# Performance work log

Measured on AMD Instinct MI355X. Metric: run time of the kernel, lower is better.

## Reference

```python
import jax, jax.numpy as jnp
import numpy as np

B, T, D, H, O = 64, 512, 64, 512, 64

def setup_inputs() -> dict:
    key = jax.random.key(0)
    ks = jax.random.split(key, 12)
    s = lambda fan: 1.0 / np.sqrt(fan)
    return {
        "x": jax.random.normal(ks[0], (B, T, D), jnp.float32),
        "W_ih0": jax.random.normal(ks[1], (4 * H, D), jnp.float32) * s(D),
        "W_hh0": jax.random.normal(ks[2], (4 * H, H), jnp.float32) * s(H),
        "b_ih0": jax.random.normal(ks[3], (4 * H,), jnp.float32) * s(H),
        "b_hh0": jax.random.normal(ks[4], (4 * H,), jnp.float32) * s(H),
        "W_ih1": jax.random.normal(ks[5], (4 * H, H), jnp.float32) * s(H),
        "W_hh1": jax.random.normal(ks[6], (4 * H, H), jnp.float32) * s(H),
        "b_ih1": jax.random.normal(ks[7], (4 * H,), jnp.float32) * s(H),
        "b_hh1": jax.random.normal(ks[8], (4 * H,), jnp.float32) * s(H),
        "lin_w": jax.random.normal(ks[9], (O, H), jnp.float32) * s(H),
        "lin_b": jax.random.normal(ks[10], (O,), jnp.float32) * s(H),
    }

def _lstm_layer(x_seq, h0, c0, W_ih, W_hh, b_ih, b_hh):
    # Precompute input contribution for all timesteps: [B, T, 4H]
    xg = jnp.einsum('btd,gd->btg', x_seq, W_ih) + b_ih
    def step(carry, xg_t):
        h, c = carry
        gates = xg_t + h @ W_hh.T + b_hh  # [B, 4H]
        i, f, g, o = jnp.split(gates, 4, axis=-1)
        i = jax.nn.sigmoid(i); f = jax.nn.sigmoid(f)
        g = jnp.tanh(g); o = jax.nn.sigmoid(o)
        c = f * c + i * g  # eval mode: dropout mask is identity
        h = o * jnp.tanh(c)
        return (h, c), h
    (h, c), ys = jax.lax.scan(step, (h0, c0), jnp.swapaxes(xg, 0, 1))
    return jnp.swapaxes(ys, 0, 1), h, c

def reference(x, W_ih0, W_hh0, b_ih0, b_hh0, W_ih1, W_hh1, b_ih1, b_hh1, lin_w, lin_b):
    h = jnp.zeros((x.shape[0], H), x.dtype)
    c = jnp.zeros((x.shape[0], H), x.dtype)
    # NOTE: faithful to source — h/c are only zeroed before layer 0 and
    # carried into layer 1 as its initial state.
    y0, h, c = _lstm_layer(x, h, c, W_ih0, W_hh0, b_ih0, b_hh0)
    y1, h, c = _lstm_layer(y0, h, c, W_ih1, W_hh1, b_ih1, b_hh1)
    return h @ lin_w.T + lin_b  # [B, O]
```

## Files before the change

### kernel.cpp

```cpp
#include <hip/hip_runtime.h>

#define TSEQ 512

typedef unsigned short us8v __attribute__((ext_vector_type(8)));
typedef __bf16 bf16x8 __attribute__((ext_vector_type(8)));
typedef float f32x4 __attribute__((ext_vector_type(4)));
typedef unsigned u32x4 __attribute__((ext_vector_type(4)));

#define OFF_FLAGS 0u
#define OFF_BIAS  524288u
#define OFF_X16   540672u
#define OFF_W0    4734976u
#define OFF_W1    7094272u
#define OFF_Y0    11288576u
#define OFF_RING  44843008u

static __device__ __forceinline__ unsigned short f2bf(float f) {
    unsigned u = __builtin_bit_cast(unsigned, f);
    u += 0x7fffu + ((u >> 16) & 1u);
    return (unsigned short)(u >> 16);
}
static __device__ __forceinline__ float sigmf(float x) { return 1.0f / (1.0f + __expf(-x)); }
static __device__ __forceinline__ float tanh_fast(float x) {
    float a = fabsf(x);
    float e = __expf(-2.0f * a);
    float t = (1.0f - e) / (1.0f + e);
    return copysignf(t, x);
}
static __device__ __forceinline__ f32x4 mfma16(us8v a, us8v b, f32x4 c) {
    return __builtin_amdgcn_mfma_f32_16x16x32_bf16(
        __builtin_bit_cast(bf16x8, a), __builtin_bit_cast(bf16x8, b), c, 0, 0, 0);
}

__global__ void setup_kernel(const float* __restrict__ x,
                             const float* __restrict__ wih0, const float* __restrict__ whh0,
                             const float* __restrict__ bih0, const float* __restrict__ bhh0,
                             const float* __restrict__ wih1, const float* __restrict__ whh1,
                             const float* __restrict__ bih1, const float* __restrict__ bhh1,
                             char* __restrict__ ws)
{
    unsigned idx = blockIdx.x * blockDim.x + threadIdx.x;
    unsigned stride = gridDim.x * blockDim.x;
    unsigned short* x16 = (unsigned short*)(ws + OFF_X16);
    unsigned short* w0  = (unsigned short*)(ws + OFF_W0);
    unsigned short* w1  = (unsigned short*)(ws + OFF_W1);
    float* bias = (float*)(ws + OFF_BIAS);
    const unsigned NX  = 64u*512u*64u;
    const unsigned NW0 = 2048u*576u;
    const unsigned NW1 = 2048u*1024u;
    const unsigned NT  = NX + NW0 + NW1 + 4096u;
    for (unsigned i = idx; i < NT; i += stride) {
        if (i < NX) {
            unsigned d = i & 63u, b = (i >> 6) & 63u, t = i >> 12;
            x16[i] = f2bf(x[((b << 9) + t) * 64u + d]);
        } else if (i < NX + NW0) {
            unsigned k = i - NX; unsigned r = k / 576u, c = k % 576u;
            float v = (c < 64u) ? wih0[r*64u + c] : whh0[r*512u + (c - 64u)];
            w0[k] = f2bf(v);
        } else if (i < NX + NW0 + NW1) {
            unsigned k = i - NX - NW0; unsigned r = k >> 10, c = k & 1023u;
            float v = (c < 512u) ? wih1[(r<<9) + c] : whh1[(r<<9) + (c - 512u)];
            w1[k] = f2bf(v);
        } else {
            unsigned k = i - NX - NW0 - NW1;
            float v = (k < 2048u) ? (bih0[k] + bhh0[k]) : (bih1[k-2048u] + bhh1[k-2048u]);
            bias[k] = v;
        }
    }
}

__launch_bounds__(256, 1)
__global__ void lstm_persist(char* __restrict__ ws)
{
    const int tid  = threadIdx.x;
    const int kq   = tid >> 6;
    const int lane = tid & 63;
    const int l15  = lane & 15;
    const int lhi  = lane >> 4;
    const int bg   = blockIdx.x & 3;
    const int hg   = blockIdx.x >> 2;

    unsigned* flags   = (unsigned*)(ws + OFF_FLAGS);
    const float* bias = (const float*)(ws + OFF_BIAS);
    const char*  x16  = ws + OFF_X16;
    char* y0   = ws + OFF_Y0;
    char* ring = ws + OFF_RING;

    __shared__ __align__(16) char zbuf[32768];
    __shared__ float gsum[4*64*18];
    __shared__ float bias_l[64];

    {
        u32x4 zz = {0u,0u,0u,0u};
        #pragma unroll
        for (int i = 0; i < 8; ++i) ((u32x4*)zbuf)[tid + i*256] = zz;
    }
    if (tid < 64) bias_l[tid] = bias[(tid >> 4)*512 + hg*16 + (tid & 15)];

    float cst = 0.0f;

    us8v A[4][8];
    {
        const char* w0p = ws + OFF_W0;
        #pragma unroll
        for (int m = 0; m < 4; ++m) {
            const char* base = w0p + (size_t)(m*512 + hg*16 + l15)*1152 + lhi*16;
            #pragma unroll
            for (int kk = 0; kk < 4; ++kk)
                A[m][kk] = *(const us8v*)(base + (2 + kq*4 + kk)*64);
            if (kq < 2) A[m][4] = *(const us8v*)(base + kq*64);
        }
    }
    __syncthreads();

    const int swzb = (l15 & 7) << 4;
    const int rb0  = l15 * 1152;
    const int rb1  = l15 * 2048;

#define POLL(WIDX) do {                                                              \
        const unsigned* fp_ = flags + (size_t)(WIDX)*128 + bg*32 + (lane & 31);      \
        unsigned fv_;                                                                \
        do {                                                                         \
            asm volatile("global_load_dword %0, %1, off sc0 sc1\n\ts_waitcnt vmcnt(0)" \
                         : "=v"(fv_) : "v"(fp_) : "memory");                         \
        } while (!__all(fv_ != 0u));                                                 \
    } while (0)

    for (int t = 0; t < TSEQ; ++t) {
        if (tid < 128) {
            int c = tid * 16, b = c >> 7, o = c & 127;
            us8v v = *(const us8v*)(x16 + (size_t)t*8192 + bg*2048 + c);
            *(us8v*)(zbuf + b*1152 + (o ^ ((b & 7) << 4))) = v;
        }
        if (t > 0) {
            POLL(t-1);
            const char* hs = y0 + ((size_t)(t-1)*4 + bg)*16384;
            #pragma unroll
            for (int i = 0; i < 4; ++i) {
                int c = tid + i*256;
                us8v v = *(const us8v*)(hs + (size_t)c*16);
                int b = c >> 6, o = (c & 63) * 16;
                *(us8v*)(zbuf + b*1152 + ((128 + o) ^ ((b & 7) << 4))) = v;
            }
        }
        __syncthreads();

        f32x4 acc[4] = {{0.f,0.f,0.f,0.f},{0.f,0.f,0.f,0.f},{0.f,0.f,0.f,0.f},{0.f,0.f,0.f,0.f}};
        #pragma unroll
        for (int kk = 0; kk < 4; ++kk) {
            us8v bf = *(const us8v*)(zbuf + rb0 + (((2 + kq*4 + kk)*64 + lhi*16) ^ swzb));
            #pragma unroll
            for (int m = 0; m < 4; ++m) acc[m] = mfma16(A[m][kk], bf, acc[m]);
        }
        if (kq < 2) {
            us8v bf = *(const us8v*)(zbuf + rb0 + ((kq*64 + lhi*16) ^ swzb));
            #pragma unroll
            for (int m = 0; m < 4; ++m) acc[m] = mfma16(A[m][4], bf, acc[m]);
        }
        #pragma unroll
        for (int m = 0; m < 4; ++m) {
            #pragma unroll
            for (int q = 0; q < 4; ++q)
                gsum[(kq*64 + m*16 + lhi*4 + q)*18 + l15] = acc[m][q];
        }
        __syncthreads();

        {
            int b = tid >> 4, p = tid & 15;
            float g4[4];
            #pragma unroll
            for (int g = 0; g < 4; ++g) {
                float s = bias_l[g*16 + p];
                #pragma unroll
                for (int kk = 0; kk < 4; ++kk) s += gsum[(kk*64 + g*16 + p)*18 + b];
                g4[g] = s;
            }
            float iv = sigmf(g4[0]), fv = sigmf(g4[1]);
            float gv = tanh_fast(g4[2]), ov = sigmf(g4[3]);
            cst = fv*cst + iv*gv;
            float h = ov * tanh_fast(cst);
            unsigned hv = f2bf(h);
            const char* dst = y0 + ((size_t)t*4 + bg)*16384 + b*1024 + (hg*16 + p)*2;
            asm volatile("global_store_short %0, %1, off sc0 sc1"
                         :: "v"(dst), "v"(hv) : "memory");
        }
        asm volatile("s_waitcnt vmcnt(0)" ::: "memory");
        __syncthreads();
        if (tid == 0) {
            unsigned one = 1;
            const unsigned* fq = flags + (size_t)t*128 + bg*32 + hg;
            asm volatile("global_store_dword %0, %1, off sc0 sc1"
                         :: "v"(fq), "v"(one) : "memory");
        }
    }

    {
        const char* w1p = ws + OFF_W1;
        #pragma unroll
        for (int m = 0; m < 4; ++m) {
            const char* base = w1p + (size_t)(m*512 + hg*16 + l15)*2048 + lhi*16;
            #pragma unroll
            for (int kk = 0; kk < 4; ++kk) {
                A[m][kk]     = *(const us8v*)(base + (kq*4 + kk)*64);
                A[m][kk + 4] = *(const us8v*)(base + (16 + kq*4 + kk)*64);
            }
        }
    }
    if (tid < 64) bias_l[tid] = bias[2048 + (tid >> 4)*512 + hg*16 + (tid & 15)];
    __syncthreads();

    for (int t = 0; t < TSEQ; ++t) {
        {
            const char* s0 = y0 + ((size_t)t*4 + bg)*16384;
            #pragma unroll
            for (int i = 0; i < 4; ++i) {
                int c = tid + i*256;
                us8v v = *(const us8v*)(s0 + (size_t)c*16);
                int b = c >> 6, o = (c & 63) * 16;
                *(us8v*)(zbuf + b*2048 + (o ^ ((b & 7) << 4))) = v;
            }
        }
        __syncthreads();

        f32x4 acc[4] = {{0.f,0.f,0.f,0.f},{0.f,0.f,0.f,0.f},{0.f,0.f,0.f,0.f},{0.f,0.f,0.f,0.f}};
        #pragma unroll
        for (int kk = 0; kk < 4; ++kk) {
            us8v bf = *(const us8v*)(zbuf + rb1 + (((kq*4 + kk)*64 + lhi*16) ^ swzb));
            #pragma unroll
            for (int m = 0; m < 4; ++m) acc[m] = mfma16(A[m][kk], bf, acc[m]);
        }
        {
            const int widx = (t == 0) ? 511 : (511 + t);
            POLL(widx);
            const char* s1 = (t == 0) ? (y0 + ((size_t)511*4 + bg)*16384)
                                      : (ring + ((size_t)((t-1) & 1)*4 + bg)*16384);
            u32x4 d0, d1, d2, d3;
            const char* a0 = s1 + (size_t)tid*16;
            const char* a1 = s1 + (size_t)(tid + 256)*16;
            const char* a2 = s1 + (size_t)(tid + 512)*16;
            const char* a3 = s1 + (size_t)(tid + 768)*16;
            asm volatile("global_load_dwordx4 %0, %4, off sc0 sc1\n\t"
                         "global_load_dwordx4 %1, %5, off sc0 sc1\n\t"
                         "global_load_dwordx4 %2, %6, off sc0 sc1\n\t"
                         "global_load_dwordx4 %3, %7, off sc0 sc1\n\t"
                         "s_waitcnt vmcnt(0)"
                         : "=&v"(d0), "=&v"(d1), "=&v"(d2), "=&v"(d3)
                         : "v"(a0), "v"(a1), "v"(a2), "v"(a3) : "memory");
            int c0i = tid, c1i = tid + 256, c2i = tid + 512, c3i = tid + 768;
            *(u32x4*)(zbuf + (c0i >> 6)*2048 + ((1024 + (c0i & 63)*16) ^ (((c0i >> 6) & 7) << 4))) = d0;
            *(u32x4*)(zbuf + (c1i >> 6)*2048 + ((1024 + (c1i & 63)*16) ^ (((c1i >> 6) & 7) << 4))) = d1;
            *(u32x4*)(zbuf + (c2i >> 6)*2048 + ((1024 + (c2i & 63)*16) ^ (((c2i >> 6) & 7) << 4))) = d2;
            *(u32x4*)(zbuf + (c3i >> 6)*2048 + ((1024 + (c3i & 63)*16) ^ (((c3i >> 6) & 7) << 4))) = d3;
        }
        __syncthreads();

        #pragma unroll
        for (int kk = 0; kk < 4; ++kk) {
            us8v bf = *(const us8v*)(zbuf + rb1 + (((16 + kq*4 + kk)*64 + lhi*16) ^ swzb));
            #pragma unroll
            for (int m = 0; m < 4; ++m) acc[m] = mfma16(A[m][kk + 4], bf, acc[m]);
        }
        #pragma unroll
        for (int m = 0; m < 4; ++m) {
            #pragma unroll
            for (int q = 0; q < 4; ++q)
                gsum[(kq*64 + m*16 + lhi*4 + q)*18 + l15] = acc[m][q];
        }
        __syncthreads();

        {
            int b = tid >> 4, p = tid & 15;
            float g4[4];
            #pragma unroll
            for (int g = 0; g < 4; ++g) {
                float s = bias_l[g*16 + p];
                #pragma unroll
                for (int kk = 0; kk < 4; ++kk) s += gsum[(kk*64 + g*16 + p)*18 + b];
                g4[g] = s;
            }
            float iv = sigmf(g4[0]), fv = sigmf(g4[1]);
            float gv = tanh_fast(g4[2]), ov = sigmf(g4[3]);
            cst = fv*cst + iv*gv;
            float h = ov * tanh_fast(cst);
            unsigned hv = f2bf(h);
            const char* dst = ring + ((size_t)(t & 1)*4 + bg)*16384 + b*1024 + (hg*16 + p)*2;
            asm volatile("global_store_short %0, %1, off sc0 sc1"
                         :: "v"(dst), "v"(hv) : "memory");
        }
        asm volatile("s_waitcnt vmcnt(0)" ::: "memory");
        __syncthreads();
        if (tid == 0) {
            unsigned one = 1;
            const unsigned* fq = flags + (size_t)(512 + t)*128 + bg*32 + hg;
            asm volatile("global_store_dword %0, %1, off sc0 sc1"
                         :: "v"(fq), "v"(one) : "memory");
        }
    }
#undef POLL
}

__global__ void final_linear(const char* __restrict__ ws,
                             const float* __restrict__ linw, const float* __restrict__ linb,
                             float* __restrict__ out)
{
    __shared__ float hrow[512];
    int b = blockIdx.x;
    int o = threadIdx.x;
    int bg = b >> 4, bl = b & 15;
    const char* src = ws + OFF_RING + ((size_t)1*4 + bg)*16384 + (size_t)bl*1024;
    {
        us8v v = *(const us8v*)(src + o*16);
        #pragma unroll
        for (int p = 0; p < 8; ++p)
            hrow[o*8+p] = __builtin_bit_cast(float, ((unsigned)v[p]) << 16);
    }
    __syncthreads();
    float acc = linb[o];
    const float* wrow = linw + o*512;
    #pragma unroll 8
    for (int k = 0; k < 512; ++k) acc += hrow[k] * wrow[k];
    out[b*64 + o] = acc;
}

extern "C" void kernel_launch(void* const* d_in, const int* in_sizes, int n_in,
                              void* d_out, int out_size, void* d_ws, size_t ws_size,
                              hipStream_t stream)
{
    const float* x    = (const float*)d_in[0];
    const float* wih0 = (const float*)d_in[1];
    const float* whh0 = (const float*)d_in[2];
    const float* bih0 = (const float*)d_in[3];
    const float* bhh0 = (const float*)d_in[4];
    const float* wih1 = (const float*)d_in[5];
    const float* whh1 = (const float*)d_in[6];
    const float* bih1 = (const float*)d_in[7];
    const float* bhh1 = (const float*)d_in[8];
    const float* linw = (const float*)d_in[9];
    const float* linb = (const float*)d_in[10];
    char* ws = (char*)d_ws;

    (void)hipMemsetAsync(ws + OFF_FLAGS, 0, 524288, stream);
    hipLaunchKernelGGL(setup_kernel, dim3(1024), dim3(256), 0, stream,
                       x, wih0, whh0, bih0, bhh0, wih1, whh1, bih1, bhh1, ws);
    hipLaunchKernelGGL(lstm_persist, dim3(128), dim3(256), 0, stream, ws);
    hipLaunchKernelGGL(final_linear, dim3(64), dim3(64), 0, stream,
                       ws, linw, linb, (float*)d_out);
}
```

Measured before the change: 2.573 ms.

## Load MFMA B-fragments directly from global memory, dropping LDS staging

Removes the shared-memory staging buffer for x, h and y0 and has each lane load its MFMA B-operand fragment straight from global memory, which removes one __syncthreads per step and the LDS write/read round trip. In layer 1 the ring loads are issued asynchronously and overlap with the y0 MFMAs. Activation stores are packed in pairs via a shuffle into dword stores, and the gsum layout is changed. In exchange, each lane now does scattered 16-byte global loads per step that rely on cache hits, and the removed barriers leave the gsum reuse ordering to the remaining barriers.

```diff
diff --git a/kernel.cpp b/kernel.cpp
--- a/kernel.cpp
+++ b/kernel.cpp
@@ -86,15 +86,9 @@
     char* y0   = ws + OFF_Y0;
     char* ring = ws + OFF_RING;
 
-    __shared__ __align__(16) char zbuf[32768];
-    __shared__ float gsum[4*64*18];
+    __shared__ float gsum[64 * 68];
     __shared__ float bias_l[64];
 
-    {
-        u32x4 zz = {0u,0u,0u,0u};
-        #pragma unroll
-        for (int i = 0; i < 8; ++i) ((u32x4*)zbuf)[tid + i*256] = zz;
-    }
     if (tid < 64) bias_l[tid] = bias[(tid >> 4)*512 + hg*16 + (tid & 15)];
 
     float cst = 0.0f;
@@ -113,9 +107,7 @@
     }
     __syncthreads();
 
-    const int swzb = (l15 & 7) << 4;
-    const int rb0  = l15 * 1152;
-    const int rb1  = l15 * 2048;
+    const int fragoff = l15*1024 + kq*256 + lhi*16;
 
 #define POLL(WIDX) do {                                                              \
         const unsigned* fp_ = flags + (size_t)(WIDX)*128 + bg*32 + (lane & 31);      \
@@ -126,64 +118,66 @@
         } while (!__all(fv_ != 0u));                                                 \
     } while (0)
 
+#define ACTIVATION_STORE(DSTBASE) do {                                               \
+        int b_ = tid >> 4, p_ = tid & 15;                                            \
+        float g4_[4];                                                                \
+        _Pragma("unroll")                                                            \
+        for (int g = 0; g < 4; ++g) {                                                \
+            float s_ = bias_l[g*16 + p_];                                            \
+            _Pragma("unroll")                                                        \
+            for (int kk = 0; kk < 4; ++kk) s_ += gsum[(g*16 + p_)*68 + kk*17 + b_];  \
+            g4_[g] = s_;                                                             \
+        }                                                                            \
+        float iv_ = sigmf(g4_[0]), fv_ = sigmf(g4_[1]);                              \
+        float gv_ = tanh_fast(g4_[2]), ov_ = sigmf(g4_[3]);                          \
+        cst = fv_*cst + iv_*gv_;                                                     \
+        float h_ = ov_ * tanh_fast(cst);                                             \
+        unsigned hv_ = f2bf(h_);                                                     \
+        unsigned pk_ = (hv_ & 0xffffu) | (((unsigned)__shfl_xor((int)hv_, 1)) << 16);\
+        if (!(p_ & 1)) {                                                             \
+            const char* dst_ = (DSTBASE) + b_*1024 + (hg*16 + p_)*2;                 \
+            asm volatile("global_store_dword %0, %1, off sc0 sc1"                    \
+                         :: "v"(dst_), "v"(pk_) : "memory");                         \
+        }                                                                            \
+    } while (0)
+
     for (int t = 0; t < TSEQ; ++t) {
-        if (tid < 128) {
-            int c = tid * 16, b = c >> 7, o = c & 127;
-            us8v v = *(const us8v*)(x16 + (size_t)t*8192 + bg*2048 + c);
-            *(us8v*)(zbuf + b*1152 + (o ^ ((b & 7) << 4))) = v;
-        }
+        us8v xf = {};
+        if (kq < 2)
+            xf = *(const us8v*)(x16 + (size_t)t*8192 + (bg*16 + l15)*128 + kq*64 + lhi*16);
+
+        f32x4 acc[4] = {{0.f,0.f,0.f,0.f},{0.f,0.f,0.f,0.f},{0.f,0.f,0.f,0.f},{0.f,0.f,0.f,0.f}};
         if (t > 0) {
             POLL(t-1);
-            const char* hs = y0 + ((size_t)(t-1)*4 + bg)*16384;
-            #pragma unroll
-            for (int i = 0; i < 4; ++i) {
-                int c = tid + i*256;
-                us8v v = *(const us8v*)(hs + (size_t)c*16);
-                int b = c >> 6, o = (c & 63) * 16;
-                *(us8v*)(zbuf + b*1152 + ((128 + o) ^ ((b & 7) << 4))) = v;
+            const char* hb = y0 + ((size_t)(t-1)*4 + bg)*16384 + fragoff;
+            us8v hf0 = *(const us8v*)(hb);
+            us8v hf1 = *(const us8v*)(hb + 64);
+            us8v hf2 = *(const us8v*)(hb + 128);
+            us8v hf3 = *(const us8v*)(hb + 192);
+            if (kq < 2) {
+                #pragma unroll
+                for (int m = 0; m < 4; ++m) acc[m] = mfma16(A[m][4], xf, acc[m]);
             }
+            #pragma unroll
+            for (int m = 0; m < 4; ++m) acc[m] = mfma16(A[m][0], hf0, acc[m]);
+            #pragma unroll
+            for (int m = 0; m < 4; ++m) acc[m] = mfma16(A[m][1], hf1, acc[m]);
+            #pragma unroll
+            for (int m = 0; m < 4; ++m) acc[m] = mfma16(A[m][2], hf2, acc[m]);
+            #pragma unroll
+            for (int m = 0; m < 4; ++m) acc[m] = mfma16(A[m][3], hf3, acc[m]);
+        } else if (kq < 2) {
+            #pragma unroll
+            for (int m = 0; m < 4; ++m) acc[m] = mfma16(A[m][4], xf, acc[m]);
+        }
+        #pragma unroll
+        for (int m = 0; m < 4; ++m) {
+            #pragma unroll
+            for (int q = 0; q < 4; ++q)
+                gsum[(m*16 + lhi*4 + q)*68 + kq*17 + l15] = acc[m][q];
         }
         __syncthreads();
-
-        f32x4 acc[4] = {{0.f,0.f,0.f,0.f},{0.f,0.f,0.f,0.f},{0.f,0.f,0.f,0.f},{0.f,0.f,0.f,0.f}};
-        #pragma unroll
-        for (int kk = 0; kk < 4; ++kk) {
-            us8v bf = *(const us8v*)(zbuf + rb0 + (((2 + kq*4 + kk)*64 + lhi*16) ^ swzb));
-            #pragma unroll
-            for (int m = 0; m < 4; ++m) acc[m] = mfma16(A[m][kk], bf, acc[m]);
-        }
-        if (kq < 2) {
-            us8v bf = *(const us8v*)(zbuf + rb0 + ((kq*64 + lhi*16) ^ swzb));
-            #pragma unroll
-            for (int m = 0; m < 4; ++m) acc[m] = mfma16(A[m][4], bf, acc[m]);
-        }
-        #pragma unroll
-        for (int m = 0; m < 4; ++m) {
-            #pragma unroll
-            for (int q = 0; q < 4; ++q)
-                gsum[(kq*64 + m*16 + lhi*4 + q)*18 + l15] = acc[m][q];
-        }
-        __syncthreads();
-
-        {
-            int b = tid >> 4, p = tid & 15;
-            float g4[4];
-            #pragma unroll
-            for (int g = 0; g < 4; ++g) {
-                float s = bias_l[g*16 + p];
-                #pragma unroll
-                for (int kk = 0; kk < 4; ++kk) s += gsum[(kk*64 + g*16 + p)*18 + b];
-                g4[g] = s;
-            }
-            float iv = sigmf(g4[0]), fv = sigmf(g4[1]);
-            float gv = tanh_fast(g4[2]), ov = sigmf(g4[3]);
-            cst = fv*cst + iv*gv;
-            float h = ov * tanh_fast(cst);
-            unsigned hv = f2bf(h);
-            const char* dst = y0 + ((size_t)t*4 + bg)*16384 + b*1024 + (hg*16 + p)*2;
-            asm volatile("global_store_short %0, %1, off sc0 sc1"
-                         :: "v"(dst), "v"(hv) : "memory");
-        }
+        ACTIVATION_STORE(y0 + ((size_t)t*4 + bg)*16384);
         asm volatile("s_waitcnt vmcnt(0)" ::: "memory");
         __syncthreads();
         if (tid == 0) {
@@ -210,83 +204,63 @@
     __syncthreads();
 
     for (int t = 0; t < TSEQ; ++t) {
+        const char* yb = y0 + ((size_t)t*4 + bg)*16384 + fragoff;
+        us8v yf0 = *(const us8v*)(yb);
+        us8v yf1 = *(const us8v*)(yb + 64);
+        us8v yf2 = *(const us8v*)(yb + 128);
+        us8v yf3 = *(const us8v*)(yb + 192);
+
+        POLL(t == 0 ? 511 : 511 + t);
+
+        const char* s1 = ((t == 0) ? (y0 + ((size_t)511*4 + bg)*16384)
+                                   : (ring + ((size_t)((t-1) & 1)*4 + bg)*16384)) + fragoff;
+        u32x4 r0, r1, r2, r3;
         {
-            const char* s0 = y0 + ((size_t)t*4 + bg)*16384;
-            #pragma unroll
-            for (int i = 0; i < 4; ++i) {
-                int c = tid + i*256;
-                us8v v = *(const us8v*)(s0 + (size_t)c*16);
-                int b = c >> 6, o = (c & 63) * 16;
-                *(us8v*)(zbuf + b*2048 + (o ^ ((b & 7) << 4))) = v;
-            }
+            const char* a0 = s1;
+            const char* a1 = s1 + 64;
+            const char* a2 = s1 + 128;
+            const char* a3 = s1 + 192;
+            asm volatile("global_load_dwordx4 %0, %1, off sc0 sc1"
+                         : "=v"(r0) : "v"(a0) : "memory");
+            asm volatile("global_load_dwordx4 %0, %1, off sc0 sc1"
+                         : "=v"(r1) : "v"(a1) : "memory");
+            asm volatile("global_load_dwordx4 %0, %1, off sc0 sc1"
+                         : "=v"(r2) : "v"(a2) : "memory");
+            asm volatile("global_load_dwordx4 %0, %1, off sc0 sc1"
+                         : "=v"(r3) : "v"(a3) : "memory");
+        }
+
+        f32x4 acc[4] = {{0.f,0.f,0.f,0.f},{0.f,0.f,0.f,0.f},{0.f,0.f,0.f,0.f},{0.f,0.f,0.f,0.f}};
+        #pragma unroll
+        for (int m = 0; m < 4; ++m) acc[m] = mfma16(A[m][0], yf0, acc[m]);
+        #pragma unroll
+        for (int m = 0; m < 4; ++m) acc[m] = mfma16(A[m][1], yf1, acc[m]);
+        #pragma unroll
+        for (int m = 0; m < 4; ++m) acc[m] = mfma16(A[m][2], yf2, acc[m]);
+        #pragma unroll
+        for (int m = 0; m < 4; ++m) acc[m] = mfma16(A[m][3], yf3, acc[m]);
+
+        asm volatile("s_waitcnt vmcnt(0)"
+                     : "+v"(r0), "+v"(r1), "+v"(r2), "+v"(r3) :: "memory");
+        __builtin_amdgcn_sched_barrier(0);
+
+        #pragma unroll
+        for (int m = 0; m < 4; ++m) acc[m] = mfma16(A[m][4], __builtin_bit_cast(us8v, r0), acc[m]);
+        #pragma unroll
+        for (int m = 0; m < 4; ++m) acc[m] = mfma16(A[m][5], __builtin_bit_cast(us8v, r1), acc[m]);
+        #pragma unroll
+        for (int m = 0; m < 4; ++m) acc[m] = mfma16(A[m][6], __builtin_bit_cast(us8v, r2), acc[m]);
+        #pragma unroll
+        for (int m = 0; m < 4; ++m) acc[m] = mfma16(A[m][7], __builtin_bit_cast(us8v, r3), acc[m]);
+
+        #pragma unroll
+        for (int m = 0; m < 4; ++m) {
+            #pragma unroll
+            for (int q = 0; q < 4; ++q)
+                gsum[(m*16 + lhi*4 + q)*68 + kq*17 + l15] = acc[m][q];
         }
         __syncthreads();
-
-        f32x4 acc[4] = {{0.f,0.f,0.f,0.f},{0.f,0.f,0.f,0.f},{0.f,0.f,0.f,0.f},{0.f,0.f,0.f,0.f}};
-        #pragma unroll
-        for (int kk = 0; kk < 4; ++kk) {
-            us8v bf = *(const us8v*)(zbuf + rb1 + (((kq*4 + kk)*64 + lhi*16) ^ swzb));
-            #pragma unroll
-            for (int m = 0; m < 4; ++m) acc[m] = mfma16(A[m][kk], bf, acc[m]);
-        }
-        {
-            const int widx = (t == 0) ? 511 : (511 + t);
-            POLL(widx);
-            const char* s1 = (t == 0) ? (y0 + ((size_t)511*4 + bg)*16384)
-                                      : (ring + ((size_t)((t-1) & 1)*4 + bg)*16384);
-            u32x4 d0, d1, d2, d3;
-            const char* a0 = s1 + (size_t)tid*16;
-            const char* a1 = s1 + (size_t)(tid + 256)*16;
-            const char* a2 = s1 + (size_t)(tid + 512)*16;
-            const char* a3 = s1 + (size_t)(tid + 768)*16;
-            asm volatile("global_load_dwordx4 %0, %4, off sc0 sc1\n\t"
-                         "global_load_dwordx4 %1, %5, off sc0 sc1\n\t"
-                         "global_load_dwordx4 %2, %6, off sc0 sc1\n\t"
-                         "global_load_dwordx4 %3, %7, off sc0 sc1\n\t"
-                         "s_waitcnt vmcnt(0)"
-                         : "=&v"(d0), "=&v"(d1), "=&v"(d2), "=&v"(d3)
-                         : "v"(a0), "v"(a1), "v"(a2), "v"(a3) : "memory");
-            int c0i = tid, c1i = tid + 256, c2i = tid + 512, c3i = tid + 768;
-            *(u32x4*)(zbuf + (c0i >> 6)*2048 + ((1024 + (c0i & 63)*16) ^ (((c0i >> 6) & 7) << 4))) = d0;
-            *(u32x4*)(zbuf + (c1i >> 6)*2048 + ((1024 + (c1i & 63)*16) ^ (((c1i >> 6) & 7) << 4))) = d1;
-            *(u32x4*)(zbuf + (c2i >> 6)*2048 + ((1024 + (c2i & 63)*16) ^ (((c2i >> 6) & 7) << 4))) = d2;
-            *(u32x4*)(zbuf + (c3i >> 6)*2048 + ((1024 + (c3i & 63)*16) ^ (((c3i >> 6) & 7) << 4))) = d3;
-        }
-        __syncthreads();
-
-        #pragma unroll
-        for (int kk = 0; kk < 4; ++kk) {
-            us8v bf = *(const us8v*)(zbuf + rb1 + (((16 + kq*4 + kk)*64 + lhi*16) ^ swzb));
-            #pragma unroll
-            for (int m = 0; m < 4; ++m) acc[m] = mfma16(A[m][kk + 4], bf, acc[m]);
-        }
-        #pragma unroll
-        for (int m = 0; m < 4; ++m) {
-            #pragma unroll
-            for (int q = 0; q < 4; ++q)
-                gsum[(kq*64 + m*16 + lhi*4 + q)*18 + l15] = acc[m][q];
-        }
-        __syncthreads();
-
-        {
-            int b = tid >> 4, p = tid & 15;
-            float g4[4];
-            #pragma unroll
-            for (int g = 0; g < 4; ++g) {
-                float s = bias_l[g*16 + p];
-                #pragma unroll
-                for (int kk = 0; kk < 4; ++kk) s += gsum[(kk*64 + g*16 + p)*18 + b];
-                g4[g] = s;
-            }
-            float iv = sigmf(g4[0]), fv = sigmf(g4[1]);
-            float gv = tanh_fast(g4[2]), ov = sigmf(g4[3]);
-            cst = fv*cst + iv*gv;
-            float h = ov * tanh_fast(cst);
-            unsigned hv = f2bf(h);
-            const char* dst = ring + ((size_t)(t & 1)*4 + bg)*16384 + b*1024 + (hg*16 + p)*2;
-            asm volatile("global_store_short %0, %1, off sc0 sc1"
-                         :: "v"(dst), "v"(hv) : "memory");
-        }
+        ACTIVATION_STORE(ring + ((size_t)(t & 1)*4 + bg)*16384);
         asm volatile("s_waitcnt vmcnt(0)" ::: "memory");
         __syncthreads();
         if (tid == 0) {
@@ -297,6 +271,7 @@
         }
     }
 #undef POLL
+#undef ACTIVATION_STORE
 }
 
 __global__ void final_linear(const char* __restrict__ ws,
```

New measurement: 2.603 ms. No clear change (+1.1%).
